# Optimization experiments

Measured on AMD Instinct MI355X. Metric: run time of the kernel, lower is better.

Reference implementation:

```python
import jax, jax.numpy as jnp
import numpy as np

HID = 256
N, D, K, EPOCHS = 100000, 512, 5, 2


def _lin(x, w, b):
    return x @ w.T + b


def setup_inputs() -> dict:
    key = jax.random.key(0)
    ks = jax.random.split(key, 16)
    s = 0.05
    return {
        "x0": jax.random.normal(ks[0], (N, D), jnp.float32),
        "x1": jax.random.normal(ks[1], (N, D), jnp.float32),
        "Hin0_w": jax.random.normal(ks[2], (HID, D), jnp.float32) * s,
        "Hin0_b": jax.random.normal(ks[3], (HID,), jnp.float32) * s,
        "Hin1_w": jax.random.normal(ks[4], (HID, D), jnp.float32) * s,
        "Hin1_b": jax.random.normal(ks[5], (HID,), jnp.float32) * s,
        "w0_w": jax.random.normal(ks[6], (HID, HID), jnp.float32) * s,
        "w0_b": jax.random.normal(ks[7], (HID,), jnp.float32) * s,
        "w1_w": jax.random.normal(ks[8], (HID, HID), jnp.float32) * s,
        "w1_b": jax.random.normal(ks[9], (HID,), jnp.float32) * s,
        "w2_w": jax.random.normal(ks[10], (HID, HID), jnp.float32) * s,
        "w2_b": jax.random.normal(ks[11], (HID,), jnp.float32) * s,
        "edge0": jax.random.randint(ks[12], (2, N * K), 0, N, dtype=jnp.int32),
        "edge1": jax.random.randint(ks[13], (2, N * K), 0, N, dtype=jnp.int32),
        "k": K,
        "update_epoch": EPOCHS,
    }


def reference(x0, x1, Hin0_w, Hin0_b, Hin1_w, Hin1_b, w0_w, w0_b,
              w1_w, w1_b, w2_w, w2_b, edge0, edge1, k, update_epoch):
    xs = (x0, x1)
    edges = (edge0, edge1)
    Hws = ((Hin0_w, Hin0_b), (Hin1_w, Hin1_b))
    n_views = len(xs)

    # per-view input projections: h_init[v] = H_ins[v](train_view[v])
    h_inits = [_lin(x, w, b) for x, (w, b) in zip(xs, Hws)]

    finals = []
    for v in range(n_views):
        # neighbor table: node i's k neighbors are edge[1][i*k : (i+1)*k]
        nbr_idx = edges[v][1].reshape(-1, k)  # [N, k]
        # cross-view self term: mean over other views of w2(h_init_other)
        slf = _lin(h_inits[1 - v], w2_w, w2_b)  # [N, HID] (nv-1 == 1)
        h = h_inits[v]
        for _ in range(update_epoch):
            h = _lin(h, w0_w, w0_b)
            # mean_j w1(h[nbr_j]) == w1(mean_j h[nbr_j]) since w1 is affine
            nbr_mean = h[nbr_idx].mean(axis=1)  # [N, HID] gather + reduce
            h = h + _lin(nbr_mean, w1_w, w1_b) + slf
        finals.append(jax.nn.relu(h))

    # average final embeddings across views
    h_out = sum(finals) / n_views
    return h_out
```

## Files before the change

kernel.cpp:

```cpp
#include <hip/hip_runtime.h>

#define NN 100000
#define DD 512
#define HH 256
#define KNB 5

typedef __attribute__((ext_vector_type(8))) short short8v;
typedef __attribute__((ext_vector_type(4))) short short4v;
typedef __attribute__((ext_vector_type(4))) float float4v;

static __device__ __forceinline__ float bf2f(unsigned short u) {
  union { unsigned int i; float f; } c;
  c.i = ((unsigned int)u) << 16;
  return c.f;
}
static __device__ __forceinline__ unsigned short f2bf(float f) {
  union { float f; unsigned int i; } c;
  c.f = f;
  unsigned int u = c.i;
  u += 0x7FFFu + ((u >> 16) & 1u);
  return (unsigned short)(u >> 16);
}

#define GLOAD16(g, l) __builtin_amdgcn_global_load_lds( \
    (const __attribute__((address_space(1))) unsigned int*)(g), \
    (__attribute__((address_space(3))) unsigned int*)(l), 16, 0, 0)

__global__ void cvt2(const float* __restrict__ s0, short* __restrict__ d0,
                     const float* __restrict__ s1, short* __restrict__ d1) {
  const int S1 = (HH * DD) / 4;
  int i = blockIdx.x * blockDim.x + threadIdx.x;
  if (i >= 2 * S1) return;
  const float* s = (i < S1) ? s0 : s1;
  short* d = (i < S1) ? d0 : d1;
  int j = (i < S1) ? i : i - S1;
  float4 v = reinterpret_cast<const float4*>(s)[j];
  short4v o;
  o[0] = (short)f2bf(v.x); o[1] = (short)f2bf(v.y);
  o[2] = (short)f2bf(v.z); o[3] = (short)f2bf(v.w);
  reinterpret_cast<short4v*>(d)[j] = o;
}

__global__ void prep_w01(const float* __restrict__ w0, const float* __restrict__ w1,
                         const float* __restrict__ w2, const float* __restrict__ b0,
                         const float* __restrict__ b1, const float* __restrict__ b2,
                         short* __restrict__ Bcat, float* __restrict__ bc) {
  int i = blockIdx.x;
  int j = threadIdx.x;
  Bcat[(size_t)i * 768 + j]       = (short)f2bf(w0[i * 256 + j]);
  Bcat[(size_t)i * 768 + 512 + j] = (short)f2bf(w2[i * 256 + j]);
  float acc = 0.f;
  for (int k = 0; k < 256; ++k)
    acc = fmaf(w1[i * 256 + k], w0[k * 256 + j], acc);
  Bcat[(size_t)i * 768 + 256 + j] = (short)f2bf(acc);
  if (j == 0) {
    float s = b0[i] + b1[i] + b2[i];
    for (int k = 0; k < 256; ++k) s = fmaf(w1[i * 256 + k], b0[k], s);
    bc[i] = s;
  }
}

template<int KD, int MODE, int EPI>
__global__ __launch_bounds__(512, 4) void gemm_k(
    const float* __restrict__ Af, const short* __restrict__ Hin,
    const short* __restrict__ Hoth, const short* __restrict__ Bw,
    const float* __restrict__ bias, short* __restrict__ Cb,
    float* __restrict__ Cf, const short* __restrict__ Fin,
    const int* __restrict__ nbr)
{
  constexpr int BM = 128;
  constexpr int BK = 64;
  __shared__ __align__(16) char BsRaw[256 * BK * 2];
  __shared__ __align__(16) char AsRaw[MODE == 0 ? BM * BK * 4 : BM * BK * 2];
  __shared__ int nbrL[MODE == 1 ? BM * KNB : 4];

  const int tid = threadIdx.x;
  const int lane = tid & 63;
  const int wave = tid >> 6;
  const int wr = wave >> 2;
  const int wc = wave & 3;
  const int row0 = blockIdx.x * BM;

  if constexpr (MODE == 1) {
    for (int e = tid; e < BM * KNB; e += 512) {
      int r = e / KNB;
      int rg = min(row0 + r, NN - 1);
      nbrL[e] = nbr[rg * KNB + (e - r * KNB)];
    }
  }

  float4v acc[4][4];
#pragma unroll
  for (int m = 0; m < 4; ++m)
#pragma unroll
    for (int n = 0; n < 4; ++n) acc[m][n] = (float4v)0.f;

  for (int k0 = 0; k0 < KD; k0 += BK) {
#pragma unroll
    for (int q = 0; q < 4; ++q) {
      int ch = q * 512 + tid;
      int r = ch >> 3, pc = ch & 7;
      int lc = pc ^ (r & 7);
      GLOAD16(Bw + (size_t)r * KD + k0 + lc * 8, BsRaw + (q * 512 + wave * 64) * 16);
    }
    if constexpr (MODE == 0) {
#pragma unroll
      for (int q = 0; q < 4; ++q) {
        int ch = q * 512 + tid;
        int r = ch >> 4, pc = ch & 15;
        int lc = pc ^ (r & 15);
        int rg = min(row0 + r, NN - 1);
        GLOAD16(Af + (size_t)rg * KD + k0 + lc * 4, AsRaw + (q * 512 + wave * 64) * 16);
      }
    } else {
      if (k0 < 256 || k0 >= 512) {
        const short* H = (k0 < 256) ? (Hin + k0) : (Hoth + (k0 - 512));
#pragma unroll
        for (int q = 0; q < 2; ++q) {
          int ch = q * 512 + tid;
          int r = ch >> 3, pc = ch & 7;
          int lc = pc ^ (r & 7);
          int rg = min(row0 + r, NN - 1);
          GLOAD16(H + (size_t)rg * HH + lc * 8, AsRaw + (q * 512 + wave * 64) * 16);
        }
      } else {
        const int kb = k0 - 256;
#pragma unroll
        for (int q = 0; q < 2; ++q) {
          int ch = q * 512 + tid;
          int r = ch >> 3, pc = ch & 7;
          int lc = pc ^ (r & 7);
          float a8[8] = {0.f, 0.f, 0.f, 0.f, 0.f, 0.f, 0.f, 0.f};
#pragma unroll
          for (int j = 0; j < KNB; ++j) {
            int id = nbrL[r * KNB + j];
            short8v v = *reinterpret_cast<const short8v*>(Hin + (size_t)id * HH + kb + lc * 8);
#pragma unroll
            for (int x = 0; x < 8; ++x) a8[x] += bf2f((unsigned short)v[x]);
          }
          short8v o;
#pragma unroll
          for (int x = 0; x < 8; ++x) o[x] = (short)f2bf(a8[x] * 0.2f);
          *reinterpret_cast<short8v*>(AsRaw + ch * 16) = o;
        }
      }
    }
    __syncthreads();

#pragma unroll
    for (int kk = 0; kk < 2; ++kk) {
      const int ckb = kk * 4 + (lane >> 4);
      short8v a[4], b[4];
#pragma unroll
      for (int n = 0; n < 4; ++n) {
        int rb = wc * 64 + n * 16 + (lane & 15);
        b[n] = *reinterpret_cast<const short8v*>(BsRaw + rb * 128 + ((ckb ^ (rb & 7)) << 4));
      }
      if constexpr (MODE == 0) {
#pragma unroll
        for (int m = 0; m < 4; ++m) {
          int ra = wr * 64 + m * 16 + (lane & 15);
          int ck0 = kk * 8 + (lane >> 4) * 2;
          float4v f0 = *reinterpret_cast<const float4v*>(AsRaw + ra * 256 + ((ck0 ^ (ra & 15)) << 4));
          float4v f1 = *reinterpret_cast<const float4v*>(AsRaw + ra * 256 + (((ck0 + 1) ^ (ra & 15)) << 4));
          short8v av;
          av[0] = (short)f2bf(f0[0]); av[1] = (short)f2bf(f0[1]);
          av[2] = (short)f2bf(f0[2]); av[3] = (short)f2bf(f0[3]);
          av[4] = (short)f2bf(f1[0]); av[5] = (short)f2bf(f1[1]);
          av[6] = (short)f2bf(f1[2]); av[7] = (short)f2bf(f1[3]);
          a[m] = av;
        }
      } else {
#pragma unroll
        for (int m = 0; m < 4; ++m) {
          int ra = wr * 64 + m * 16 + (lane & 15);
          a[m] = *reinterpret_cast<const short8v*>(AsRaw + ra * 128 + ((ckb ^ (ra & 7)) << 4));
        }
      }
#pragma unroll
      for (int m = 0; m < 4; ++m)
#pragma unroll
        for (int n = 0; n < 4; ++n)
          acc[m][n] = __builtin_amdgcn_mfma_f32_16x16x32_bf16(b[n], a[m], acc[m][n], 0, 0, 0);
    }
    __syncthreads();
  }

  const int crow = lane & 15;
  const int cg = (lane >> 4) * 4;
#pragma unroll
  for (int m = 0; m < 4; ++m) {
    int rg = row0 + wr * 64 + m * 16 + crow;
    if (rg >= NN) continue;
#pragma unroll
    for (int n = 0; n < 4; ++n) {
      int colb = wc * 64 + n * 16 + cg;
      size_t off = (size_t)rg * HH + colb;
      float4v bi = *reinterpret_cast<const float4v*>(bias + colb);
      float v[4];
#pragma unroll
      for (int i = 0; i < 4; ++i) v[i] = acc[m][n][i] + bi[i];
      if constexpr (EPI >= 2) {
#pragma unroll
        for (int i = 0; i < 4; ++i) v[i] = fmaxf(v[i], 0.f);
      }
      if constexpr (EPI <= 2) {
        short4v o;
#pragma unroll
        for (int i = 0; i < 4; ++i) o[i] = (short)f2bf(v[i]);
        *reinterpret_cast<short4v*>(Cb + off) = o;
      } else {
        short4v f4 = *reinterpret_cast<const short4v*>(Fin + off);
        float4v o;
#pragma unroll
        for (int i = 0; i < 4; ++i) o[i] = (v[i] + bf2f((unsigned short)f4[i])) * 0.5f;
        *reinterpret_cast<float4v*>(Cf + off) = o;
      }
    }
  }
}

extern "C" void kernel_launch(void* const* d_in, const int* in_sizes, int n_in,
                              void* d_out, int out_size, void* d_ws, size_t ws_size,
                              hipStream_t stream) {
  const float* x0  = (const float*)d_in[0];
  const float* x1  = (const float*)d_in[1];
  const float* wh0 = (const float*)d_in[2];
  const float* bh0 = (const float*)d_in[3];
  const float* wh1 = (const float*)d_in[4];
  const float* bh1 = (const float*)d_in[5];
  const float* w0  = (const float*)d_in[6];
  const float* b0  = (const float*)d_in[7];
  const float* w1  = (const float*)d_in[8];
  const float* b1  = (const float*)d_in[9];
  const float* w2  = (const float*)d_in[10];
  const float* b2  = (const float*)d_in[11];
  const int* e0    = (const int*)d_in[12];
  const int* e1    = (const int*)d_in[13];
  const int* nbr0  = e0 + (size_t)NN * KNB;
  const int* nbr1  = e1 + (size_t)NN * KNB;
  float* out       = (float*)d_out;

  char* ws = (char*)d_ws;
  size_t off = 0;
  auto alloc = [&](size_t bytes) -> void* {
    off = (off + 255) & ~(size_t)255;
    void* p = ws + off;
    off += bytes;
    return p;
  };

  short* Wh0  = (short*)alloc((size_t)HH * DD * 2);
  short* Wh1  = (short*)alloc((size_t)HH * DD * 2);
  short* Bcat = (short*)alloc((size_t)HH * 768 * 2);
  float* bc   = (float*)alloc((size_t)HH * 4);
  const size_t NB = (size_t)NN * HH * 2;
  short* hi0 = (short*)alloc(NB);
  short* hi1 = (short*)alloc(NB);
  short* hb  = (short*)alloc(NB);
  short* f0  = (short*)alloc(NB);

  cvt2<<<dim3(256), dim3(256), 0, stream>>>(wh0, Wh0, wh1, Wh1);
  prep_w01<<<dim3(256), dim3(256), 0, stream>>>(w0, w1, w2, b0, b1, b2, Bcat, bc);

  dim3 blk(512);
  dim3 gg((NN + 127) / 128);

  gemm_k<DD, 0, 0><<<gg, blk, 0, stream>>>(x0, nullptr, nullptr, Wh0, bh0, hi0, nullptr, nullptr, nullptr);
  gemm_k<DD, 0, 0><<<gg, blk, 0, stream>>>(x1, nullptr, nullptr, Wh1, bh1, hi1, nullptr, nullptr, nullptr);

  gemm_k<768, 1, 0><<<gg, blk, 0, stream>>>(nullptr, hi0, hi1, Bcat, bc, hb, nullptr, nullptr, nbr0);
  gemm_k<768, 1, 2><<<gg, blk, 0, stream>>>(nullptr, hb, hi1, Bcat, bc, f0, nullptr, nullptr, nbr0);

  gemm_k<768, 1, 0><<<gg, blk, 0, stream>>>(nullptr, hi1, hi0, Bcat, bc, hb, nullptr, nullptr, nbr1);
  gemm_k<768, 1, 3><<<gg, blk, 0, stream>>>(nullptr, hb, hi0, Bcat, bc, nullptr, out, f0, nbr1);

  (void)in_sizes; (void)n_in; (void)out_size; (void)ws_size;
}
```

Before: 540.5 us.

## Merge both views into dual-view epoch kernels and batch the input projections

The two view projections now run in a single launch that uses a 2D grid. Each epoch step handles both views in one kernel: blocks of 64 rows share one pass over the weight tile, with half the waves computing view 0 and half view 1. The final step averages the two ReLU outputs through shared memory, so the bf16 f0 intermediate no longer goes to and from global memory. This cuts the launch count and the repeated weight-tile loads. In exchange, tiles are smaller (64 rows per view), each block does more gather work, and the launch_bounds occupancy hint is gone.

```diff
diff --git a/kernel.cpp b/kernel.cpp
--- a/kernel.cpp
+++ b/kernel.cpp
@@ -60,34 +60,26 @@
   }
 }
 
-template<int KD, int MODE, int EPI>
-__global__ __launch_bounds__(512, 4) void gemm_k(
-    const float* __restrict__ Af, const short* __restrict__ Hin,
-    const short* __restrict__ Hoth, const short* __restrict__ Bw,
-    const float* __restrict__ bias, short* __restrict__ Cb,
-    float* __restrict__ Cf, const short* __restrict__ Fin,
-    const int* __restrict__ nbr)
+__global__ __launch_bounds__(512) void proj_k(
+    const float* __restrict__ Af0, const float* __restrict__ Af1,
+    const short* __restrict__ Bw0, const short* __restrict__ Bw1,
+    const float* __restrict__ bi0, const float* __restrict__ bi1,
+    short* __restrict__ Cb0, short* __restrict__ Cb1)
 {
-  constexpr int BM = 128;
-  constexpr int BK = 64;
-  __shared__ __align__(16) char BsRaw[256 * BK * 2];
-  __shared__ __align__(16) char AsRaw[MODE == 0 ? BM * BK * 4 : BM * BK * 2];
-  __shared__ int nbrL[MODE == 1 ? BM * KNB : 4];
+  const float* Af = blockIdx.y ? Af1 : Af0;
+  const short* Bw = blockIdx.y ? Bw1 : Bw0;
+  const float* bias = blockIdx.y ? bi1 : bi0;
+  short* Cb = blockIdx.y ? Cb1 : Cb0;
+
+  __shared__ __align__(16) char BsRaw[256 * 64 * 2];
+  __shared__ __align__(16) char AsRaw[128 * 64 * 4];
 
   const int tid = threadIdx.x;
   const int lane = tid & 63;
   const int wave = tid >> 6;
   const int wr = wave >> 2;
   const int wc = wave & 3;
-  const int row0 = blockIdx.x * BM;
-
-  if constexpr (MODE == 1) {
-    for (int e = tid; e < BM * KNB; e += 512) {
-      int r = e / KNB;
-      int rg = min(row0 + r, NN - 1);
-      nbrL[e] = nbr[rg * KNB + (e - r * KNB)];
-    }
-  }
+  const int row0 = blockIdx.x * 128;
 
   float4v acc[4][4];
 #pragma unroll
@@ -95,55 +87,21 @@
 #pragma unroll
     for (int n = 0; n < 4; ++n) acc[m][n] = (float4v)0.f;
 
-  for (int k0 = 0; k0 < KD; k0 += BK) {
+  for (int k0 = 0; k0 < DD; k0 += 64) {
 #pragma unroll
     for (int q = 0; q < 4; ++q) {
       int ch = q * 512 + tid;
       int r = ch >> 3, pc = ch & 7;
       int lc = pc ^ (r & 7);
-      GLOAD16(Bw + (size_t)r * KD + k0 + lc * 8, BsRaw + (q * 512 + wave * 64) * 16);
-    }
-    if constexpr (MODE == 0) {
-#pragma unroll
-      for (int q = 0; q < 4; ++q) {
-        int ch = q * 512 + tid;
-        int r = ch >> 4, pc = ch & 15;
-        int lc = pc ^ (r & 15);
-        int rg = min(row0 + r, NN - 1);
-        GLOAD16(Af + (size_t)rg * KD + k0 + lc * 4, AsRaw + (q * 512 + wave * 64) * 16);
-      }
-    } else {
-      if (k0 < 256 || k0 >= 512) {
-        const short* H = (k0 < 256) ? (Hin + k0) : (Hoth + (k0 - 512));
-#pragma unroll
-        for (int q = 0; q < 2; ++q) {
-          int ch = q * 512 + tid;
-          int r = ch >> 3, pc = ch & 7;
-          int lc = pc ^ (r & 7);
-          int rg = min(row0 + r, NN - 1);
-          GLOAD16(H + (size_t)rg * HH + lc * 8, AsRaw + (q * 512 + wave * 64) * 16);
-        }
-      } else {
-        const int kb = k0 - 256;
-#pragma unroll
-        for (int q = 0; q < 2; ++q) {
-          int ch = q * 512 + tid;
-          int r = ch >> 3, pc = ch & 7;
-          int lc = pc ^ (r & 7);
-          float a8[8] = {0.f, 0.f, 0.f, 0.f, 0.f, 0.f, 0.f, 0.f};
-#pragma unroll
-          for (int j = 0; j < KNB; ++j) {
-            int id = nbrL[r * KNB + j];
-            short8v v = *reinterpret_cast<const short8v*>(Hin + (size_t)id * HH + kb + lc * 8);
-#pragma unroll
-            for (int x = 0; x < 8; ++x) a8[x] += bf2f((unsigned short)v[x]);
-          }
-          short8v o;
-#pragma unroll
-          for (int x = 0; x < 8; ++x) o[x] = (short)f2bf(a8[x] * 0.2f);
-          *reinterpret_cast<short8v*>(AsRaw + ch * 16) = o;
-        }
-      }
+      GLOAD16(Bw + (size_t)r * DD + k0 + lc * 8, BsRaw + (q * 512 + wave * 64) * 16);
+    }
+#pragma unroll
+    for (int q = 0; q < 4; ++q) {
+      int ch = q * 512 + tid;
+      int r = ch >> 4, pc = ch & 15;
+      int lc = pc ^ (r & 15);
+      int rg = min(row0 + r, NN - 1);
+      GLOAD16(Af + (size_t)rg * DD + k0 + lc * 4, AsRaw + (q * 512 + wave * 64) * 16);
     }
     __syncthreads();
 
@@ -156,26 +114,18 @@
         int rb = wc * 64 + n * 16 + (lane & 15);
         b[n] = *reinterpret_cast<const short8v*>(BsRaw + rb * 128 + ((ckb ^ (rb & 7)) << 4));
       }
-      if constexpr (MODE == 0) {
-#pragma unroll
-        for (int m = 0; m < 4; ++m) {
-          int ra = wr * 64 + m * 16 + (lane & 15);
-          int ck0 = kk * 8 + (lane >> 4) * 2;
-          float4v f0 = *reinterpret_cast<const float4v*>(AsRaw + ra * 256 + ((ck0 ^ (ra & 15)) << 4));
-          float4v f1 = *reinterpret_cast<const float4v*>(AsRaw + ra * 256 + (((ck0 + 1) ^ (ra & 15)) << 4));
-          short8v av;
-          av[0] = (short)f2bf(f0[0]); av[1] = (short)f2bf(f0[1]);
-          av[2] = (short)f2bf(f0[2]); av[3] = (short)f2bf(f0[3]);
-          av[4] = (short)f2bf(f1[0]); av[5] = (short)f2bf(f1[1]);
-          av[6] = (short)f2bf(f1[2]); av[7] = (short)f2bf(f1[3]);
-          a[m] = av;
-        }
-      } else {
-#pragma unroll
-        for (int m = 0; m < 4; ++m) {
-          int ra = wr * 64 + m * 16 + (lane & 15);
-          a[m] = *reinterpret_cast<const short8v*>(AsRaw + ra * 128 + ((ckb ^ (ra & 7)) << 4));
-        }
+#pragma unroll
+      for (int m = 0; m < 4; ++m) {
+        int ra = wr * 64 + m * 16 + (lane & 15);
+        int ck0 = kk * 8 + (lane >> 4) * 2;
+        float4v f0 = *reinterpret_cast<const float4v*>(AsRaw + ra * 256 + ((ck0 ^ (ra & 15)) << 4));
+        float4v f1 = *reinterpret_cast<const float4v*>(AsRaw + ra * 256 + (((ck0 + 1) ^ (ra & 15)) << 4));
+        short8v av;
+        av[0] = (short)f2bf(f0[0]); av[1] = (short)f2bf(f0[1]);
+        av[2] = (short)f2bf(f0[2]); av[3] = (short)f2bf(f0[3]);
+        av[4] = (short)f2bf(f1[0]); av[5] = (short)f2bf(f1[1]);
+        av[6] = (short)f2bf(f1[2]); av[7] = (short)f2bf(f1[3]);
+        a[m] = av;
       }
 #pragma unroll
       for (int m = 0; m < 4; ++m)
@@ -197,24 +147,173 @@
       int colb = wc * 64 + n * 16 + cg;
       size_t off = (size_t)rg * HH + colb;
       float4v bi = *reinterpret_cast<const float4v*>(bias + colb);
-      float v[4];
-#pragma unroll
-      for (int i = 0; i < 4; ++i) v[i] = acc[m][n][i] + bi[i];
-      if constexpr (EPI >= 2) {
-#pragma unroll
-        for (int i = 0; i < 4; ++i) v[i] = fmaxf(v[i], 0.f);
-      }
-      if constexpr (EPI <= 2) {
+      short4v o;
+#pragma unroll
+      for (int i = 0; i < 4; ++i) o[i] = (short)f2bf(acc[m][n][i] + bi[i]);
+      *reinterpret_cast<short4v*>(Cb + off) = o;
+    }
+  }
+}
+
+template<int EPI>
+__global__ __launch_bounds__(512) void epoch_dual(
+    const short* __restrict__ D0, const short* __restrict__ D1,
+    const short* __restrict__ C0, const short* __restrict__ C1,
+    const short* __restrict__ Bw, const float* __restrict__ bias,
+    short* __restrict__ O0, short* __restrict__ O1, float* __restrict__ Of,
+    const int* __restrict__ nbr0, const int* __restrict__ nbr1)
+{
+  __shared__ __align__(16) char BsRaw[256 * 64 * 2];
+  __shared__ __align__(16) char A0Raw[64 * 64 * 2];
+  __shared__ __align__(16) char A1Raw[64 * 64 * 2];
+  __shared__ int nbrL[2][64][KNB];
+
+  const int tid = threadIdx.x;
+  const int lane = tid & 63;
+  const int wave = tid >> 6;
+  const int vv = wave >> 2;
+  const int wc = wave & 3;
+  const int row0 = blockIdx.x * 64;
+
+  for (int e = tid; e < 2 * 64 * KNB; e += 512) {
+    int v = e / (64 * KNB);
+    int r = (e / KNB) & 63;
+    int rg = min(row0 + r, NN - 1);
+    const int* nb = v ? nbr1 : nbr0;
+    nbrL[v][r][e % KNB] = nb[rg * KNB + (e % KNB)];
+  }
+
+  float4v acc[4][4];
+#pragma unroll
+  for (int m = 0; m < 4; ++m)
+#pragma unroll
+    for (int n = 0; n < 4; ++n) acc[m][n] = (float4v)0.f;
+
+  for (int s = 0; s < 12; ++s) {
+    const int k0 = s * 64;
+#pragma unroll
+    for (int q = 0; q < 4; ++q) {
+      int ch = q * 512 + tid;
+      int r = ch >> 3, pc = ch & 7;
+      int lc = pc ^ (r & 7);
+      GLOAD16(Bw + (size_t)r * 768 + k0 + lc * 8, BsRaw + (q * 512 + wave * 64) * 16);
+    }
+    {
+      int ch = tid;
+      int r = ch >> 3, pc = ch & 7;
+      int lc = pc ^ (r & 7);
+      if (s < 4 || s >= 8) {
+        const short* S0 = (s < 4) ? (D0 + k0) : (C0 + (k0 - 512));
+        const short* S1 = (s < 4) ? (D1 + k0) : (C1 + (k0 - 512));
+        int rg = min(row0 + r, NN - 1);
+        GLOAD16(S0 + (size_t)rg * HH + lc * 8, A0Raw + (wave * 64) * 16);
+        GLOAD16(S1 + (size_t)rg * HH + lc * 8, A1Raw + (wave * 64) * 16);
+      } else {
+        const int kb = k0 - 256;
+        float a0[8] = {0.f,0.f,0.f,0.f,0.f,0.f,0.f,0.f};
+        float a1[8] = {0.f,0.f,0.f,0.f,0.f,0.f,0.f,0.f};
+#pragma unroll
+        for (int j = 0; j < KNB; ++j) {
+          int id0 = nbrL[0][r][j];
+          int id1 = nbrL[1][r][j];
+          short8v v0 = *reinterpret_cast<const short8v*>(D0 + (size_t)id0 * HH + kb + lc * 8);
+          short8v v1 = *reinterpret_cast<const short8v*>(D1 + (size_t)id1 * HH + kb + lc * 8);
+#pragma unroll
+          for (int x = 0; x < 8; ++x) {
+            a0[x] += bf2f((unsigned short)v0[x]);
+            a1[x] += bf2f((unsigned short)v1[x]);
+          }
+        }
+        short8v o0, o1;
+#pragma unroll
+        for (int x = 0; x < 8; ++x) {
+          o0[x] = (short)f2bf(a0[x] * 0.2f);
+          o1[x] = (short)f2bf(a1[x] * 0.2f);
+        }
+        *reinterpret_cast<short8v*>(A0Raw + ch * 16) = o0;
+        *reinterpret_cast<short8v*>(A1Raw + ch * 16) = o1;
+      }
+    }
+    __syncthreads();
+
+    const char* Asrc = vv ? A1Raw : A0Raw;
+#pragma unroll
+    for (int kk = 0; kk < 2; ++kk) {
+      const int ckb = kk * 4 + (lane >> 4);
+      short8v a[4], b[4];
+#pragma unroll
+      for (int n = 0; n < 4; ++n) {
+        int rb = wc * 64 + n * 16 + (lane & 15);
+        b[n] = *reinterpret_cast<const short8v*>(BsRaw + rb * 128 + ((ckb ^ (rb & 7)) << 4));
+      }
+#pragma unroll
+      for (int m = 0; m < 4; ++m) {
+        int ra = m * 16 + (lane & 15);
+        a[m] = *reinterpret_cast<const short8v*>(Asrc + ra * 128 + ((ckb ^ (ra & 7)) << 4));
+      }
+#pragma unroll
+      for (int m = 0; m < 4; ++m)
+#pragma unroll
+        for (int n = 0; n < 4; ++n)
+          acc[m][n] = __builtin_amdgcn_mfma_f32_16x16x32_bf16(b[n], a[m], acc[m][n], 0, 0, 0);
+    }
+    __syncthreads();
+  }
+
+  const int crow = lane & 15;
+  const int cg = (lane >> 4) * 4;
+  if constexpr (EPI == 0) {
+    short* O = vv ? O1 : O0;
+#pragma unroll
+    for (int m = 0; m < 4; ++m) {
+      int rg = row0 + m * 16 + crow;
+      if (rg >= NN) continue;
+#pragma unroll
+      for (int n = 0; n < 4; ++n) {
+        int colb = wc * 64 + n * 16 + cg;
+        float4v bi = *reinterpret_cast<const float4v*>(bias + colb);
         short4v o;
 #pragma unroll
-        for (int i = 0; i < 4; ++i) o[i] = (short)f2bf(v[i]);
-        *reinterpret_cast<short4v*>(Cb + off) = o;
-      } else {
-        short4v f4 = *reinterpret_cast<const short4v*>(Fin + off);
-        float4v o;
-#pragma unroll
-        for (int i = 0; i < 4; ++i) o[i] = (v[i] + bf2f((unsigned short)f4[i])) * 0.5f;
-        *reinterpret_cast<float4v*>(Cf + off) = o;
+        for (int i = 0; i < 4; ++i) o[i] = (short)f2bf(acc[m][n][i] + bi[i]);
+        *reinterpret_cast<short4v*>(O + (size_t)rg * HH + colb) = o;
+      }
+    }
+  } else {
+    if (vv == 0) {
+#pragma unroll
+      for (int m = 0; m < 4; ++m) {
+        int rl = m * 16 + crow;
+#pragma unroll
+        for (int n = 0; n < 4; ++n) {
+          int colb = wc * 64 + n * 16 + cg;
+          float4v bi = *reinterpret_cast<const float4v*>(bias + colb);
+          short4v o;
+#pragma unroll
+          for (int i = 0; i < 4; ++i) o[i] = (short)f2bf(fmaxf(acc[m][n][i] + bi[i], 0.f));
+          int c8 = (colb >> 2) ^ (rl & 7);
+          *reinterpret_cast<short4v*>(BsRaw + rl * 512 + c8 * 8) = o;
+        }
+      }
+    }
+    __syncthreads();
+    if (vv == 1) {
+#pragma unroll
+      for (int m = 0; m < 4; ++m) {
+        int rl = m * 16 + crow;
+        int rg = row0 + rl;
+        if (rg >= NN) continue;
+#pragma unroll
+        for (int n = 0; n < 4; ++n) {
+          int colb = wc * 64 + n * 16 + cg;
+          float4v bi = *reinterpret_cast<const float4v*>(bias + colb);
+          int c8 = (colb >> 2) ^ (rl & 7);
+          short4v x4 = *reinterpret_cast<const short4v*>(BsRaw + rl * 512 + c8 * 8);
+          float4v o;
+#pragma unroll
+          for (int i = 0; i < 4; ++i)
+            o[i] = (fmaxf(acc[m][n][i] + bi[i], 0.f) + bf2f((unsigned short)x4[i])) * 0.5f;
+          *reinterpret_cast<float4v*>(Of + (size_t)rg * HH + colb) = o;
+        }
       }
     }
   }
@@ -257,23 +356,22 @@
   const size_t NB = (size_t)NN * HH * 2;
   short* hi0 = (short*)alloc(NB);
   short* hi1 = (short*)alloc(NB);
-  short* hb  = (short*)alloc(NB);
-  short* f0  = (short*)alloc(NB);
+  short* hb0 = (short*)alloc(NB);
+  short* hb1 = (short*)alloc(NB);
 
   cvt2<<<dim3(256), dim3(256), 0, stream>>>(wh0, Wh0, wh1, Wh1);
   prep_w01<<<dim3(256), dim3(256), 0, stream>>>(w0, w1, w2, b0, b1, b2, Bcat, bc);
 
-  dim3 blk(512);
-  dim3 gg((NN + 127) / 128);
-
-  gemm_k<DD, 0, 0><<<gg, blk, 0, stream>>>(x0, nullptr, nullptr, Wh0, bh0, hi0, nullptr, nullptr, nullptr);
-  gemm_k<DD, 0, 0><<<gg, blk, 0, stream>>>(x1, nullptr, nullptr, Wh1, bh1, hi1, nullptr, nullptr, nullptr);
-
-  gemm_k<768, 1, 0><<<gg, blk, 0, stream>>>(nullptr, hi0, hi1, Bcat, bc, hb, nullptr, nullptr, nbr0);
-  gemm_k<768, 1, 2><<<gg, blk, 0, stream>>>(nullptr, hb, hi1, Bcat, bc, f0, nullptr, nullptr, nbr0);
-
-  gemm_k<768, 1, 0><<<gg, blk, 0, stream>>>(nullptr, hi1, hi0, Bcat, bc, hb, nullptr, nullptr, nbr1);
-  gemm_k<768, 1, 3><<<gg, blk, 0, stream>>>(nullptr, hb, hi0, Bcat, bc, nullptr, out, f0, nbr1);
+  proj_k<<<dim3((NN + 127) / 128, 2), dim3(512), 0, stream>>>(
+      x0, x1, Wh0, Wh1, bh0, bh1, hi0, hi1);
+
+  dim3 ge((NN + 63) / 64);
+
+  epoch_dual<0><<<ge, dim3(512), 0, stream>>>(
+      hi0, hi1, hi1, hi0, Bcat, bc, hb0, hb1, nullptr, nbr0, nbr1);
+
+  epoch_dual<1><<<ge, dim3(512), 0, stream>>>(
+      hb0, hb1, hi1, hi0, Bcat, bc, nullptr, nullptr, out, nbr0, nbr1);
 
   (void)in_sizes; (void)n_in; (void)out_size; (void)ws_size;
 }
```

Result: slower. 593.2 us (+9.7%).

## Software-pipeline epoch GEMM with double-buffered A tiles and prefetched neighbor gathers

Applied to the files above, without the earlier changes.

Splits the generic GEMM into a projection kernel that handles both views in one 2D-grid launch and a dedicated epoch kernel. The epoch kernel double-buffers the A tile in LDS and, while computing the current K-step, prefetches the next A tile or issues the next neighbor gathers into registers. Explicit waitcnt and barrier scheduling replace the plain syncthreads. The aim is to hide global and gather latency behind MFMA work. The cost is higher register pressure from the held gather results, plus a second hb buffer so both views' first epochs can run back to back.

```diff
diff --git a/kernel.cpp b/kernel.cpp
--- a/kernel.cpp
+++ b/kernel.cpp
@@ -60,34 +60,26 @@
   }
 }
 
-template<int KD, int MODE, int EPI>
-__global__ __launch_bounds__(512, 4) void gemm_k(
-    const float* __restrict__ Af, const short* __restrict__ Hin,
-    const short* __restrict__ Hoth, const short* __restrict__ Bw,
-    const float* __restrict__ bias, short* __restrict__ Cb,
-    float* __restrict__ Cf, const short* __restrict__ Fin,
-    const int* __restrict__ nbr)
+__global__ __launch_bounds__(512) void proj_k(
+    const float* __restrict__ Af0, const float* __restrict__ Af1,
+    const short* __restrict__ Bw0, const short* __restrict__ Bw1,
+    const float* __restrict__ bi0, const float* __restrict__ bi1,
+    short* __restrict__ Cb0, short* __restrict__ Cb1)
 {
-  constexpr int BM = 128;
-  constexpr int BK = 64;
-  __shared__ __align__(16) char BsRaw[256 * BK * 2];
-  __shared__ __align__(16) char AsRaw[MODE == 0 ? BM * BK * 4 : BM * BK * 2];
-  __shared__ int nbrL[MODE == 1 ? BM * KNB : 4];
+  const float* Af = blockIdx.y ? Af1 : Af0;
+  const short* Bw = blockIdx.y ? Bw1 : Bw0;
+  const float* bias = blockIdx.y ? bi1 : bi0;
+  short* Cb = blockIdx.y ? Cb1 : Cb0;
+
+  __shared__ __align__(16) char BsRaw[256 * 64 * 2];
+  __shared__ __align__(16) char AsRaw[128 * 64 * 4];
 
   const int tid = threadIdx.x;
   const int lane = tid & 63;
   const int wave = tid >> 6;
   const int wr = wave >> 2;
   const int wc = wave & 3;
-  const int row0 = blockIdx.x * BM;
-
-  if constexpr (MODE == 1) {
-    for (int e = tid; e < BM * KNB; e += 512) {
-      int r = e / KNB;
-      int rg = min(row0 + r, NN - 1);
-      nbrL[e] = nbr[rg * KNB + (e - r * KNB)];
-    }
-  }
+  const int row0 = blockIdx.x * 128;
 
   float4v acc[4][4];
 #pragma unroll
@@ -95,55 +87,21 @@
 #pragma unroll
     for (int n = 0; n < 4; ++n) acc[m][n] = (float4v)0.f;
 
-  for (int k0 = 0; k0 < KD; k0 += BK) {
+  for (int k0 = 0; k0 < DD; k0 += 64) {
 #pragma unroll
     for (int q = 0; q < 4; ++q) {
       int ch = q * 512 + tid;
       int r = ch >> 3, pc = ch & 7;
       int lc = pc ^ (r & 7);
-      GLOAD16(Bw + (size_t)r * KD + k0 + lc * 8, BsRaw + (q * 512 + wave * 64) * 16);
-    }
-    if constexpr (MODE == 0) {
-#pragma unroll
-      for (int q = 0; q < 4; ++q) {
-        int ch = q * 512 + tid;
-        int r = ch >> 4, pc = ch & 15;
-        int lc = pc ^ (r & 15);
-        int rg = min(row0 + r, NN - 1);
-        GLOAD16(Af + (size_t)rg * KD + k0 + lc * 4, AsRaw + (q * 512 + wave * 64) * 16);
-      }
-    } else {
-      if (k0 < 256 || k0 >= 512) {
-        const short* H = (k0 < 256) ? (Hin + k0) : (Hoth + (k0 - 512));
-#pragma unroll
-        for (int q = 0; q < 2; ++q) {
-          int ch = q * 512 + tid;
-          int r = ch >> 3, pc = ch & 7;
-          int lc = pc ^ (r & 7);
-          int rg = min(row0 + r, NN - 1);
-          GLOAD16(H + (size_t)rg * HH + lc * 8, AsRaw + (q * 512 + wave * 64) * 16);
-        }
-      } else {
-        const int kb = k0 - 256;
-#pragma unroll
-        for (int q = 0; q < 2; ++q) {
-          int ch = q * 512 + tid;
-          int r = ch >> 3, pc = ch & 7;
-          int lc = pc ^ (r & 7);
-          float a8[8] = {0.f, 0.f, 0.f, 0.f, 0.f, 0.f, 0.f, 0.f};
-#pragma unroll
-          for (int j = 0; j < KNB; ++j) {
-            int id = nbrL[r * KNB + j];
-            short8v v = *reinterpret_cast<const short8v*>(Hin + (size_t)id * HH + kb + lc * 8);
-#pragma unroll
-            for (int x = 0; x < 8; ++x) a8[x] += bf2f((unsigned short)v[x]);
-          }
-          short8v o;
-#pragma unroll
-          for (int x = 0; x < 8; ++x) o[x] = (short)f2bf(a8[x] * 0.2f);
-          *reinterpret_cast<short8v*>(AsRaw + ch * 16) = o;
-        }
-      }
+      GLOAD16(Bw + (size_t)r * DD + k0 + lc * 8, BsRaw + (q * 512 + wave * 64) * 16);
+    }
+#pragma unroll
+    for (int q = 0; q < 4; ++q) {
+      int ch = q * 512 + tid;
+      int r = ch >> 4, pc = ch & 15;
+      int lc = pc ^ (r & 15);
+      int rg = min(row0 + r, NN - 1);
+      GLOAD16(Af + (size_t)rg * DD + k0 + lc * 4, AsRaw + (q * 512 + wave * 64) * 16);
     }
     __syncthreads();
 
@@ -156,26 +114,18 @@
         int rb = wc * 64 + n * 16 + (lane & 15);
         b[n] = *reinterpret_cast<const short8v*>(BsRaw + rb * 128 + ((ckb ^ (rb & 7)) << 4));
       }
-      if constexpr (MODE == 0) {
-#pragma unroll
-        for (int m = 0; m < 4; ++m) {
-          int ra = wr * 64 + m * 16 + (lane & 15);
-          int ck0 = kk * 8 + (lane >> 4) * 2;
-          float4v f0 = *reinterpret_cast<const float4v*>(AsRaw + ra * 256 + ((ck0 ^ (ra & 15)) << 4));
-          float4v f1 = *reinterpret_cast<const float4v*>(AsRaw + ra * 256 + (((ck0 + 1) ^ (ra & 15)) << 4));
-          short8v av;
-          av[0] = (short)f2bf(f0[0]); av[1] = (short)f2bf(f0[1]);
-          av[2] = (short)f2bf(f0[2]); av[3] = (short)f2bf(f0[3]);
-          av[4] = (short)f2bf(f1[0]); av[5] = (short)f2bf(f1[1]);
-          av[6] = (short)f2bf(f1[2]); av[7] = (short)f2bf(f1[3]);
-          a[m] = av;
-        }
-      } else {
-#pragma unroll
-        for (int m = 0; m < 4; ++m) {
-          int ra = wr * 64 + m * 16 + (lane & 15);
-          a[m] = *reinterpret_cast<const short8v*>(AsRaw + ra * 128 + ((ckb ^ (ra & 7)) << 4));
-        }
+#pragma unroll
+      for (int m = 0; m < 4; ++m) {
+        int ra = wr * 64 + m * 16 + (lane & 15);
+        int ck0 = kk * 8 + (lane >> 4) * 2;
+        float4v f0 = *reinterpret_cast<const float4v*>(AsRaw + ra * 256 + ((ck0 ^ (ra & 15)) << 4));
+        float4v f1 = *reinterpret_cast<const float4v*>(AsRaw + ra * 256 + (((ck0 + 1) ^ (ra & 15)) << 4));
+        short8v av;
+        av[0] = (short)f2bf(f0[0]); av[1] = (short)f2bf(f0[1]);
+        av[2] = (short)f2bf(f0[2]); av[3] = (short)f2bf(f0[3]);
+        av[4] = (short)f2bf(f1[0]); av[5] = (short)f2bf(f1[1]);
+        av[6] = (short)f2bf(f1[2]); av[7] = (short)f2bf(f1[3]);
+        a[m] = av;
       }
 #pragma unroll
       for (int m = 0; m < 4; ++m)
@@ -185,6 +135,167 @@
     }
     __syncthreads();
   }
+
+  const int crow = lane & 15;
+  const int cg = (lane >> 4) * 4;
+#pragma unroll
+  for (int m = 0; m < 4; ++m) {
+    int rg = row0 + wr * 64 + m * 16 + crow;
+    if (rg >= NN) continue;
+#pragma unroll
+    for (int n = 0; n < 4; ++n) {
+      int colb = wc * 64 + n * 16 + cg;
+      size_t off = (size_t)rg * HH + colb;
+      float4v bi = *reinterpret_cast<const float4v*>(bias + colb);
+      short4v o;
+#pragma unroll
+      for (int i = 0; i < 4; ++i) o[i] = (short)f2bf(acc[m][n][i] + bi[i]);
+      *reinterpret_cast<short4v*>(Cb + off) = o;
+    }
+  }
+}
+
+
+#define EPOCH_STEP(S, WN, PF) { \
+  _Pragma("unroll") \
+  for (int q = 0; q < 4; ++q) { \
+    int ch = q * 512 + tid; \
+    int r = ch >> 3, pc = ch & 7; \
+    int lc = pc ^ (r & 7); \
+    GLOAD16(Bw + (size_t)r * 768 + (S) * 64 + lc * 8, BsRaw + (q * 512 + wave * 64) * 16); \
+  } \
+  __builtin_amdgcn_sched_barrier(0); \
+  { \
+    char* Anx = AsRaw + (((S) & 1) ^ 1) * 16384; \
+    if constexpr ((PF) == 0) { \
+      constexpr int SN = (S) + 1; \
+      const short* Ps = (SN < 4) ? (D + SN * 64) : (Cc + (SN * 64 - 512)); \
+      _Pragma("unroll") \
+      for (int q = 0; q < 2; ++q) { \
+        int ch = q * 512 + tid; \
+        int r = ch >> 3; \
+        int lc = (ch & 7) ^ (r & 7); \
+        int rg = min(row0 + r, NN - 1); \
+        GLOAD16(Ps + (size_t)rg * HH + lc * 8, Anx + (q * 512 + wave * 64) * 16); \
+      } \
+    } else if constexpr ((PF) == 1) { \
+      constexpr int KB = ((S) + 1) * 64 - 256; \
+      const short* Dk = D + KB + lc0 * 8; \
+      _Pragma("unroll") \
+      for (int j = 0; j < KNB; ++j) { \
+        gA[j] = *reinterpret_cast<const short8v*>(Dk + (size_t)nbrL[r0][j] * HH); \
+        gB[j] = *reinterpret_cast<const short8v*>(Dk + (size_t)nbrL[r0 + 64][j] * HH); \
+      } \
+    } \
+    __builtin_amdgcn_sched_barrier(0); \
+    asm volatile("s_waitcnt vmcnt(" #WN ")" ::: "memory"); \
+    __builtin_amdgcn_sched_barrier(0); \
+    __builtin_amdgcn_s_barrier(); \
+    { \
+      const char* Ac = AsRaw + ((S) & 1) * 16384; \
+      _Pragma("unroll") \
+      for (int kk = 0; kk < 2; ++kk) { \
+        const int ckb = kk * 4 + (lane >> 4); \
+        short8v a[4], b[4]; \
+        _Pragma("unroll") \
+        for (int n = 0; n < 4; ++n) { \
+          int rb = wc * 64 + n * 16 + (lane & 15); \
+          b[n] = *reinterpret_cast<const short8v*>(BsRaw + rb * 128 + ((ckb ^ (rb & 7)) << 4)); \
+        } \
+        _Pragma("unroll") \
+        for (int m = 0; m < 4; ++m) { \
+          int ra = wr * 64 + m * 16 + (lane & 15); \
+          a[m] = *reinterpret_cast<const short8v*>(Ac + ra * 128 + ((ckb ^ (ra & 7)) << 4)); \
+        } \
+        _Pragma("unroll") \
+        for (int m = 0; m < 4; ++m) \
+          _Pragma("unroll") \
+          for (int n = 0; n < 4; ++n) \
+            acc[m][n] = __builtin_amdgcn_mfma_f32_16x16x32_bf16(b[n], a[m], acc[m][n], 0, 0, 0); \
+      } \
+    } \
+    if constexpr ((PF) == 1) { \
+      asm volatile("s_waitcnt vmcnt(0)" ::: "memory"); \
+      __builtin_amdgcn_sched_barrier(0); \
+      float s0[8] = {0,0,0,0,0,0,0,0}, s1[8] = {0,0,0,0,0,0,0,0}; \
+      _Pragma("unroll") \
+      for (int j = 0; j < KNB; ++j) \
+        _Pragma("unroll") \
+        for (int x = 0; x < 8; ++x) { \
+          s0[x] += bf2f((unsigned short)gA[j][x]); \
+          s1[x] += bf2f((unsigned short)gB[j][x]); \
+        } \
+      short8v o0, o1; \
+      _Pragma("unroll") \
+      for (int x = 0; x < 8; ++x) { \
+        o0[x] = (short)f2bf(s0[x] * 0.2f); \
+        o1[x] = (short)f2bf(s1[x] * 0.2f); \
+      } \
+      *reinterpret_cast<short8v*>(Anx + tid * 16) = o0; \
+      *reinterpret_cast<short8v*>(Anx + (tid + 512) * 16) = o1; \
+    } \
+  } \
+  asm volatile("s_waitcnt lgkmcnt(0)" ::: "memory"); \
+  __builtin_amdgcn_sched_barrier(0); \
+  __builtin_amdgcn_s_barrier(); \
+}
+
+template<int EPI>
+__global__ __launch_bounds__(512, 4) void epoch_pipe(
+    const short* __restrict__ D, const short* __restrict__ Cc,
+    const short* __restrict__ Bw, const float* __restrict__ bias,
+    short* __restrict__ Ob, float* __restrict__ Of,
+    const short* __restrict__ Fin, const int* __restrict__ nbr)
+{
+  __shared__ __align__(16) char BsRaw[256 * 64 * 2];
+  __shared__ __align__(16) char AsRaw[2 * 128 * 64 * 2];
+  __shared__ int nbrL[128][KNB];
+
+  const int tid = threadIdx.x;
+  const int lane = tid & 63;
+  const int wave = tid >> 6;
+  const int wr = wave >> 2;
+  const int wc = wave & 3;
+  const int row0 = blockIdx.x * 128;
+  const int r0 = tid >> 3;
+  const int lc0 = (tid & 7) ^ (r0 & 7);
+
+  short8v gA[KNB], gB[KNB];
+
+  for (int e = tid; e < 128 * KNB; e += 512) {
+    int r = e / KNB;
+    int rg = min(row0 + r, NN - 1);
+    nbrL[r][e - r * KNB] = nbr[rg * KNB + (e - r * KNB)];
+  }
+
+  float4v acc[4][4];
+#pragma unroll
+  for (int m = 0; m < 4; ++m)
+#pragma unroll
+    for (int n = 0; n < 4; ++n) acc[m][n] = (float4v)0.f;
+
+#pragma unroll
+  for (int q = 0; q < 2; ++q) {
+    int ch = q * 512 + tid;
+    int r = ch >> 3;
+    int lc = (ch & 7) ^ (r & 7);
+    int rg = min(row0 + r, NN - 1);
+    GLOAD16(D + (size_t)rg * HH + lc * 8, AsRaw + (q * 512 + wave * 64) * 16);
+  }
+  __builtin_amdgcn_sched_barrier(0);
+
+  EPOCH_STEP(0, 2, 0)
+  EPOCH_STEP(1, 2, 0)
+  EPOCH_STEP(2, 2, 0)
+  EPOCH_STEP(3, 10, 1)
+  EPOCH_STEP(4, 10, 1)
+  EPOCH_STEP(5, 10, 1)
+  EPOCH_STEP(6, 10, 1)
+  EPOCH_STEP(7, 2, 0)
+  EPOCH_STEP(8, 2, 0)
+  EPOCH_STEP(9, 2, 0)
+  EPOCH_STEP(10, 2, 0)
+  EPOCH_STEP(11, 0, 2)
 
   const int crow = lane & 15;
   const int cg = (lane >> 4) * 4;
@@ -208,13 +319,14 @@
         short4v o;
 #pragma unroll
         for (int i = 0; i < 4; ++i) o[i] = (short)f2bf(v[i]);
-        *reinterpret_cast<short4v*>(Cb + off) = o;
+        *reinterpret_cast<short4v*>(Ob + off) = o;
       } else {
         short4v f4 = *reinterpret_cast<const short4v*>(Fin + off);
         float4v o;
 #pragma unroll
-        for (int i = 0; i < 4; ++i) o[i] = (v[i] + bf2f((unsigned short)f4[i])) * 0.5f;
-        *reinterpret_cast<float4v*>(Cf + off) = o;
+        for (int i = 0; i < 4; ++i)
+          o[i] = (v[i] + bf2f((unsigned short)f4[i])) * 0.5f;
+        *reinterpret_cast<float4v*>(Of + off) = o;
       }
     }
   }
@@ -257,23 +369,23 @@
   const size_t NB = (size_t)NN * HH * 2;
   short* hi0 = (short*)alloc(NB);
   short* hi1 = (short*)alloc(NB);
-  short* hb  = (short*)alloc(NB);
+  short* hb0 = (short*)alloc(NB);
+  short* hb1 = (short*)alloc(NB);
   short* f0  = (short*)alloc(NB);
 
   cvt2<<<dim3(256), dim3(256), 0, stream>>>(wh0, Wh0, wh1, Wh1);
   prep_w01<<<dim3(256), dim3(256), 0, stream>>>(w0, w1, w2, b0, b1, b2, Bcat, bc);
 
-  dim3 blk(512);
-  dim3 gg((NN + 127) / 128);
-
-  gemm_k<DD, 0, 0><<<gg, blk, 0, stream>>>(x0, nullptr, nullptr, Wh0, bh0, hi0, nullptr, nullptr, nullptr);
-  gemm_k<DD, 0, 0><<<gg, blk, 0, stream>>>(x1, nullptr, nullptr, Wh1, bh1, hi1, nullptr, nullptr, nullptr);
-
-  gemm_k<768, 1, 0><<<gg, blk, 0, stream>>>(nullptr, hi0, hi1, Bcat, bc, hb, nullptr, nullptr, nbr0);
-  gemm_k<768, 1, 2><<<gg, blk, 0, stream>>>(nullptr, hb, hi1, Bcat, bc, f0, nullptr, nullptr, nbr0);
-
-  gemm_k<768, 1, 0><<<gg, blk, 0, stream>>>(nullptr, hi1, hi0, Bcat, bc, hb, nullptr, nullptr, nbr1);
-  gemm_k<768, 1, 3><<<gg, blk, 0, stream>>>(nullptr, hb, hi0, Bcat, bc, nullptr, out, f0, nbr1);
+  proj_k<<<dim3((NN + 127) / 128, 2), dim3(512), 0, stream>>>(
+      x0, x1, Wh0, Wh1, bh0, bh1, hi0, hi1);
+
+  dim3 ge((NN + 127) / 128);
+
+  epoch_pipe<0><<<ge, dim3(512), 0, stream>>>(hi0, hi1, Bcat, bc, hb0, nullptr, nullptr, nbr0);
+  epoch_pipe<0><<<ge, dim3(512), 0, stream>>>(hi1, hi0, Bcat, bc, hb1, nullptr, nullptr, nbr1);
+
+  epoch_pipe<2><<<ge, dim3(512), 0, stream>>>(hb0, hi1, Bcat, bc, f0, nullptr, nullptr, nbr0);
+  epoch_pipe<3><<<ge, dim3(512), 0, stream>>>(hb1, hi0, Bcat, bc, nullptr, out, f0, nbr1);
 
   (void)in_sizes; (void)n_in; (void)out_size; (void)ws_size;
 }
```

Measured after the change: 1.004 ms. 85.7% more time.

## Double-buffer epoch GEMM with BK=32 and batch both views per launch

Applied to the files above, without the earlier changes.

Splits the generic GEMM into a projection kernel and an epoch kernel. The projection kernel covers both views in one launch through blockIdx.y. The epoch kernel shrinks the K tile to 32 and double-buffers the LDS tiles, so the next tile's loads and neighbour gather are issued before the current tile's MFMAs. The first epoch of both views is batched into one launch with separate hb buffers. This cuts launch count and overlaps the gather latency with compute, at the cost of an extra workspace buffer, more LDS per block and fewer view-2 launches combined later.

```diff
diff --git a/kernel.cpp b/kernel.cpp
--- a/kernel.cpp
+++ b/kernel.cpp
@@ -60,34 +60,26 @@
   }
 }
 
-template<int KD, int MODE, int EPI>
-__global__ __launch_bounds__(512, 4) void gemm_k(
-    const float* __restrict__ Af, const short* __restrict__ Hin,
-    const short* __restrict__ Hoth, const short* __restrict__ Bw,
-    const float* __restrict__ bias, short* __restrict__ Cb,
-    float* __restrict__ Cf, const short* __restrict__ Fin,
-    const int* __restrict__ nbr)
+__global__ __launch_bounds__(512) void proj_k(
+    const float* __restrict__ Af0, const float* __restrict__ Af1,
+    const short* __restrict__ Bw0, const short* __restrict__ Bw1,
+    const float* __restrict__ bi0, const float* __restrict__ bi1,
+    short* __restrict__ Cb0, short* __restrict__ Cb1)
 {
-  constexpr int BM = 128;
-  constexpr int BK = 64;
-  __shared__ __align__(16) char BsRaw[256 * BK * 2];
-  __shared__ __align__(16) char AsRaw[MODE == 0 ? BM * BK * 4 : BM * BK * 2];
-  __shared__ int nbrL[MODE == 1 ? BM * KNB : 4];
+  const float* Af = blockIdx.y ? Af1 : Af0;
+  const short* Bw = blockIdx.y ? Bw1 : Bw0;
+  const float* bias = blockIdx.y ? bi1 : bi0;
+  short* Cb = blockIdx.y ? Cb1 : Cb0;
+
+  __shared__ __align__(16) char BsRaw[256 * 64 * 2];
+  __shared__ __align__(16) char AsRaw[128 * 64 * 4];
 
   const int tid = threadIdx.x;
   const int lane = tid & 63;
   const int wave = tid >> 6;
   const int wr = wave >> 2;
   const int wc = wave & 3;
-  const int row0 = blockIdx.x * BM;
-
-  if constexpr (MODE == 1) {
-    for (int e = tid; e < BM * KNB; e += 512) {
-      int r = e / KNB;
-      int rg = min(row0 + r, NN - 1);
-      nbrL[e] = nbr[rg * KNB + (e - r * KNB)];
-    }
-  }
+  const int row0 = blockIdx.x * 128;
 
   float4v acc[4][4];
 #pragma unroll
@@ -95,55 +87,21 @@
 #pragma unroll
     for (int n = 0; n < 4; ++n) acc[m][n] = (float4v)0.f;
 
-  for (int k0 = 0; k0 < KD; k0 += BK) {
+  for (int k0 = 0; k0 < DD; k0 += 64) {
 #pragma unroll
     for (int q = 0; q < 4; ++q) {
       int ch = q * 512 + tid;
       int r = ch >> 3, pc = ch & 7;
       int lc = pc ^ (r & 7);
-      GLOAD16(Bw + (size_t)r * KD + k0 + lc * 8, BsRaw + (q * 512 + wave * 64) * 16);
-    }
-    if constexpr (MODE == 0) {
-#pragma unroll
-      for (int q = 0; q < 4; ++q) {
-        int ch = q * 512 + tid;
-        int r = ch >> 4, pc = ch & 15;
-        int lc = pc ^ (r & 15);
-        int rg = min(row0 + r, NN - 1);
-        GLOAD16(Af + (size_t)rg * KD + k0 + lc * 4, AsRaw + (q * 512 + wave * 64) * 16);
-      }
-    } else {
-      if (k0 < 256 || k0 >= 512) {
-        const short* H = (k0 < 256) ? (Hin + k0) : (Hoth + (k0 - 512));
-#pragma unroll
-        for (int q = 0; q < 2; ++q) {
-          int ch = q * 512 + tid;
-          int r = ch >> 3, pc = ch & 7;
-          int lc = pc ^ (r & 7);
-          int rg = min(row0 + r, NN - 1);
-          GLOAD16(H + (size_t)rg * HH + lc * 8, AsRaw + (q * 512 + wave * 64) * 16);
-        }
-      } else {
-        const int kb = k0 - 256;
-#pragma unroll
-        for (int q = 0; q < 2; ++q) {
-          int ch = q * 512 + tid;
-          int r = ch >> 3, pc = ch & 7;
-          int lc = pc ^ (r & 7);
-          float a8[8] = {0.f, 0.f, 0.f, 0.f, 0.f, 0.f, 0.f, 0.f};
-#pragma unroll
-          for (int j = 0; j < KNB; ++j) {
-            int id = nbrL[r * KNB + j];
-            short8v v = *reinterpret_cast<const short8v*>(Hin + (size_t)id * HH + kb + lc * 8);
-#pragma unroll
-            for (int x = 0; x < 8; ++x) a8[x] += bf2f((unsigned short)v[x]);
-          }
-          short8v o;
-#pragma unroll
-          for (int x = 0; x < 8; ++x) o[x] = (short)f2bf(a8[x] * 0.2f);
-          *reinterpret_cast<short8v*>(AsRaw + ch * 16) = o;
-        }
-      }
+      GLOAD16(Bw + (size_t)r * DD + k0 + lc * 8, BsRaw + (q * 512 + wave * 64) * 16);
+    }
+#pragma unroll
+    for (int q = 0; q < 4; ++q) {
+      int ch = q * 512 + tid;
+      int r = ch >> 4, pc = ch & 15;
+      int lc = pc ^ (r & 15);
+      int rg = min(row0 + r, NN - 1);
+      GLOAD16(Af + (size_t)rg * DD + k0 + lc * 4, AsRaw + (q * 512 + wave * 64) * 16);
     }
     __syncthreads();
 
@@ -156,26 +114,147 @@
         int rb = wc * 64 + n * 16 + (lane & 15);
         b[n] = *reinterpret_cast<const short8v*>(BsRaw + rb * 128 + ((ckb ^ (rb & 7)) << 4));
       }
-      if constexpr (MODE == 0) {
-#pragma unroll
-        for (int m = 0; m < 4; ++m) {
-          int ra = wr * 64 + m * 16 + (lane & 15);
-          int ck0 = kk * 8 + (lane >> 4) * 2;
-          float4v f0 = *reinterpret_cast<const float4v*>(AsRaw + ra * 256 + ((ck0 ^ (ra & 15)) << 4));
-          float4v f1 = *reinterpret_cast<const float4v*>(AsRaw + ra * 256 + (((ck0 + 1) ^ (ra & 15)) << 4));
-          short8v av;
-          av[0] = (short)f2bf(f0[0]); av[1] = (short)f2bf(f0[1]);
-          av[2] = (short)f2bf(f0[2]); av[3] = (short)f2bf(f0[3]);
-          av[4] = (short)f2bf(f1[0]); av[5] = (short)f2bf(f1[1]);
-          av[6] = (short)f2bf(f1[2]); av[7] = (short)f2bf(f1[3]);
-          a[m] = av;
+#pragma unroll
+      for (int m = 0; m < 4; ++m) {
+        int ra = wr * 64 + m * 16 + (lane & 15);
+        int ck0 = kk * 8 + (lane >> 4) * 2;
+        float4v f0 = *reinterpret_cast<const float4v*>(AsRaw + ra * 256 + ((ck0 ^ (ra & 15)) << 4));
+        float4v f1 = *reinterpret_cast<const float4v*>(AsRaw + ra * 256 + (((ck0 + 1) ^ (ra & 15)) << 4));
+        short8v av;
+        av[0] = (short)f2bf(f0[0]); av[1] = (short)f2bf(f0[1]);
+        av[2] = (short)f2bf(f0[2]); av[3] = (short)f2bf(f0[3]);
+        av[4] = (short)f2bf(f1[0]); av[5] = (short)f2bf(f1[1]);
+        av[6] = (short)f2bf(f1[2]); av[7] = (short)f2bf(f1[3]);
+        a[m] = av;
+      }
+#pragma unroll
+      for (int m = 0; m < 4; ++m)
+#pragma unroll
+        for (int n = 0; n < 4; ++n)
+          acc[m][n] = __builtin_amdgcn_mfma_f32_16x16x32_bf16(b[n], a[m], acc[m][n], 0, 0, 0);
+    }
+    __syncthreads();
+  }
+
+  const int crow = lane & 15;
+  const int cg = (lane >> 4) * 4;
+#pragma unroll
+  for (int m = 0; m < 4; ++m) {
+    int rg = row0 + wr * 64 + m * 16 + crow;
+    if (rg >= NN) continue;
+#pragma unroll
+    for (int n = 0; n < 4; ++n) {
+      int colb = wc * 64 + n * 16 + cg;
+      size_t off = (size_t)rg * HH + colb;
+      float4v bi = *reinterpret_cast<const float4v*>(bias + colb);
+      short4v o;
+#pragma unroll
+      for (int i = 0; i < 4; ++i) o[i] = (short)f2bf(acc[m][n][i] + bi[i]);
+      *reinterpret_cast<short4v*>(Cb + off) = o;
+    }
+  }
+}
+
+template<int EPI>
+__global__ __launch_bounds__(512) void epoch2(
+    const short* __restrict__ D0_, const short* __restrict__ C0_,
+    short* __restrict__ O0_, const int* __restrict__ n0_,
+    const short* __restrict__ D1_, const short* __restrict__ C1_,
+    short* __restrict__ O1_, const int* __restrict__ n1_,
+    const short* __restrict__ Bw, const float* __restrict__ bias,
+    float* __restrict__ Of, const short* __restrict__ Fin)
+{
+  __shared__ __align__(16) char BsRaw[2 * 16384];
+  __shared__ __align__(16) char AsRaw[2 * 8192];
+  __shared__ int nbrL[128][KNB];
+
+  const short* D  = blockIdx.y ? D1_ : D0_;
+  const short* Cc = blockIdx.y ? C1_ : C0_;
+  short* Ob       = blockIdx.y ? O1_ : O0_;
+  const int* nbr  = blockIdx.y ? n1_ : n0_;
+
+  const int tid = threadIdx.x;
+  const int lane = tid & 63;
+  const int wave = tid >> 6;
+  const int wr = wave >> 2;
+  const int wc = wave & 3;
+  const int row0 = blockIdx.x * 128;
+
+  for (int e = tid; e < 128 * KNB; e += 512) {
+    int r = e / KNB;
+    int rg = min(row0 + r, NN - 1);
+    nbrL[r][e - r * KNB] = nbr[rg * KNB + (e - r * KNB)];
+  }
+
+  {
+#pragma unroll
+    for (int q = 0; q < 2; ++q) {
+      int ch = q * 512 + tid;
+      int r = ch >> 2, pc = ch & 3;
+      int lc = pc ^ ((r >> 1) & 3);
+      GLOAD16(Bw + (size_t)r * 768 + lc * 8, BsRaw + (q * 512 + wave * 64) * 16);
+    }
+    int r = tid >> 2, pc = tid & 3;
+    int lc = pc ^ ((r >> 1) & 3);
+    int rg = min(row0 + r, NN - 1);
+    GLOAD16(D + (size_t)rg * HH + lc * 8, AsRaw + (wave * 64) * 16);
+  }
+  __syncthreads();
+
+  float4v acc[4][4];
+#pragma unroll
+  for (int m = 0; m < 4; ++m)
+#pragma unroll
+    for (int n = 0; n < 4; ++n) acc[m][n] = (float4v)0.f;
+
+  for (int s = 0; s < 24; ++s) {
+    const int sn = s + 1;
+    if (sn < 24) {
+      char* Bn = BsRaw + (sn & 1) * 16384;
+#pragma unroll
+      for (int q = 0; q < 2; ++q) {
+        int ch = q * 512 + tid;
+        int r = ch >> 2, pc = ch & 3;
+        int lc = pc ^ ((r >> 1) & 3);
+        GLOAD16(Bw + (size_t)r * 768 + sn * 32 + lc * 8, Bn + (q * 512 + wave * 64) * 16);
+      }
+      char* An = AsRaw + (sn & 1) * 8192;
+      int r = tid >> 2, pc = tid & 3;
+      int lc = pc ^ ((r >> 1) & 3);
+      if (sn < 8 || sn >= 16) {
+        const short* Ps = (sn < 8) ? (D + sn * 32) : (Cc + (sn * 32 - 512));
+        int rg = min(row0 + r, NN - 1);
+        GLOAD16(Ps + (size_t)rg * HH + lc * 8, An + (wave * 64) * 16);
+      } else {
+        const int kb = sn * 32 - 256;
+        const short* Dk = D + kb + lc * 8;
+        float a8[8] = {0.f, 0.f, 0.f, 0.f, 0.f, 0.f, 0.f, 0.f};
+#pragma unroll
+        for (int j = 0; j < KNB; ++j) {
+          short8v v = *reinterpret_cast<const short8v*>(Dk + (size_t)nbrL[r][j] * HH);
+#pragma unroll
+          for (int x = 0; x < 8; ++x) a8[x] += bf2f((unsigned short)v[x]);
         }
-      } else {
-#pragma unroll
-        for (int m = 0; m < 4; ++m) {
-          int ra = wr * 64 + m * 16 + (lane & 15);
-          a[m] = *reinterpret_cast<const short8v*>(AsRaw + ra * 128 + ((ckb ^ (ra & 7)) << 4));
-        }
+        short8v o;
+#pragma unroll
+        for (int x = 0; x < 8; ++x) o[x] = (short)f2bf(a8[x] * 0.2f);
+        *reinterpret_cast<short8v*>(An + tid * 16) = o;
+      }
+    }
+    {
+      const char* Bc = BsRaw + (s & 1) * 16384;
+      const char* Ac = AsRaw + (s & 1) * 8192;
+      const int ckb = lane >> 4;
+      short8v a[4], b[4];
+#pragma unroll
+      for (int n = 0; n < 4; ++n) {
+        int rb = wc * 64 + n * 16 + (lane & 15);
+        b[n] = *reinterpret_cast<const short8v*>(Bc + rb * 64 + ((ckb ^ ((rb >> 1) & 3)) << 4));
+      }
+#pragma unroll
+      for (int m = 0; m < 4; ++m) {
+        int ra = wr * 64 + m * 16 + (lane & 15);
+        a[m] = *reinterpret_cast<const short8v*>(Ac + ra * 64 + ((ckb ^ ((ra >> 1) & 3)) << 4));
       }
 #pragma unroll
       for (int m = 0; m < 4; ++m)
@@ -208,13 +287,14 @@
         short4v o;
 #pragma unroll
         for (int i = 0; i < 4; ++i) o[i] = (short)f2bf(v[i]);
-        *reinterpret_cast<short4v*>(Cb + off) = o;
+        *reinterpret_cast<short4v*>(Ob + off) = o;
       } else {
         short4v f4 = *reinterpret_cast<const short4v*>(Fin + off);
         float4v o;
 #pragma unroll
-        for (int i = 0; i < 4; ++i) o[i] = (v[i] + bf2f((unsigned short)f4[i])) * 0.5f;
-        *reinterpret_cast<float4v*>(Cf + off) = o;
+        for (int i = 0; i < 4; ++i)
+          o[i] = (v[i] + bf2f((unsigned short)f4[i])) * 0.5f;
+        *reinterpret_cast<float4v*>(Of + off) = o;
       }
     }
   }
@@ -257,23 +337,26 @@
   const size_t NB = (size_t)NN * HH * 2;
   short* hi0 = (short*)alloc(NB);
   short* hi1 = (short*)alloc(NB);
-  short* hb  = (short*)alloc(NB);
+  short* hb0 = (short*)alloc(NB);
+  short* hb1 = (short*)alloc(NB);
   short* f0  = (short*)alloc(NB);
 
   cvt2<<<dim3(256), dim3(256), 0, stream>>>(wh0, Wh0, wh1, Wh1);
   prep_w01<<<dim3(256), dim3(256), 0, stream>>>(w0, w1, w2, b0, b1, b2, Bcat, bc);
 
-  dim3 blk(512);
-  dim3 gg((NN + 127) / 128);
-
-  gemm_k<DD, 0, 0><<<gg, blk, 0, stream>>>(x0, nullptr, nullptr, Wh0, bh0, hi0, nullptr, nullptr, nullptr);
-  gemm_k<DD, 0, 0><<<gg, blk, 0, stream>>>(x1, nullptr, nullptr, Wh1, bh1, hi1, nullptr, nullptr, nullptr);
-
-  gemm_k<768, 1, 0><<<gg, blk, 0, stream>>>(nullptr, hi0, hi1, Bcat, bc, hb, nullptr, nullptr, nbr0);
-  gemm_k<768, 1, 2><<<gg, blk, 0, stream>>>(nullptr, hb, hi1, Bcat, bc, f0, nullptr, nullptr, nbr0);
-
-  gemm_k<768, 1, 0><<<gg, blk, 0, stream>>>(nullptr, hi1, hi0, Bcat, bc, hb, nullptr, nullptr, nbr1);
-  gemm_k<768, 1, 3><<<gg, blk, 0, stream>>>(nullptr, hb, hi0, Bcat, bc, nullptr, out, f0, nbr1);
+  proj_k<<<dim3((NN + 127) / 128, 2), dim3(512), 0, stream>>>(
+      x0, x1, Wh0, Wh1, bh0, bh1, hi0, hi1);
+
+  dim3 ge((NN + 127) / 128);
+
+  epoch2<0><<<dim3(ge.x, 2), dim3(512), 0, stream>>>(
+      hi0, hi1, hb0, nbr0,  hi1, hi0, hb1, nbr1,  Bcat, bc, nullptr, nullptr);
+
+  epoch2<2><<<dim3(ge.x, 1), dim3(512), 0, stream>>>(
+      hb0, hi1, f0, nbr0,   hb0, hi1, f0, nbr0,   Bcat, bc, nullptr, nullptr);
+
+  epoch2<3><<<dim3(ge.x, 1), dim3(512), 0, stream>>>(
+      hb1, hi0, nullptr, nbr1,  hb1, hi0, nullptr, nbr1,  Bcat, bc, out, f0);
 
   (void)in_sizes; (void)n_in; (void)out_size; (void)ws_size;
 }
```

Result: slower. 630.1 us (+16.6%).
